# Performance work log

Hardware: AMD Instinct MI355X
Metric: run time of the kernel (lower is better)

Reference implementation:

```python
import jax, jax.numpy as jnp
import numpy as np

N_ATOMS = 50000
N_EDGES = 600000
N_FEAT = 128      # n_atom_basis
N_FILT = 128      # n_filters
N_GAUSS = 32
N_CONV = 3
CUTOFF = 5.0
ATOMS_PER_MOL = 50
N_MOL = N_ATOMS // ATOMS_PER_MOL
N_KEYS = 2        # energy_0, energy_1
HIDDEN_RO = 64
LOG2 = float(np.log(2.0))


def ssp(x):
    # shifted softplus: softplus(x) - log(2)
    return jax.nn.softplus(x) - LOG2


def setup_inputs() -> dict:
    key = jax.random.key(0)
    ks = jax.random.split(key, 16)
    def w(k, shape, fan_in):
        return jax.random.normal(k, shape, dtype=jnp.float32) / np.sqrt(fan_in)
    return {
        "z": jax.random.randint(ks[0], (N_ATOMS,), 1, 100),
        "xyz": jax.random.normal(ks[1], (N_ATOMS, 3), dtype=jnp.float32) * 4.0,
        "nbr_list": jax.random.randint(ks[2], (N_EDGES, 2), 0, N_ATOMS),
        "mol_idx": jnp.arange(N_ATOMS, dtype=jnp.int32) // ATOMS_PER_MOL,
        "embed": jax.random.normal(ks[3], (100, N_FEAT), dtype=jnp.float32) * 0.1,
        "We1": w(ks[4], (N_CONV, N_GAUSS, N_FILT), N_GAUSS),
        "be1": jnp.zeros((N_CONV, N_FILT), jnp.float32),
        "We2": w(ks[5], (N_CONV, N_FILT, N_FILT), N_FILT),
        "be2": jnp.zeros((N_CONV, N_FILT), jnp.float32),
        "Wn": w(ks[6], (N_CONV, N_FEAT, N_FILT), N_FEAT),
        "bn": jnp.zeros((N_CONV, N_FILT), jnp.float32),
        "Wu1": w(ks[7], (N_CONV, N_FILT, N_FEAT), N_FILT),
        "bu1": jnp.zeros((N_CONV, N_FEAT), jnp.float32),
        "Wu2": w(ks[8], (N_CONV, N_FEAT, N_FEAT), N_FEAT),
        "bu2": jnp.zeros((N_CONV, N_FEAT), jnp.float32),
        "Wr1": w(ks[9], (N_KEYS, N_FEAT, HIDDEN_RO), N_FEAT),
        "br1": jnp.zeros((N_KEYS, HIDDEN_RO), jnp.float32),
        "Wr2": w(ks[10], (N_KEYS, HIDDEN_RO, 1), HIDDEN_RO),
        "br2": jnp.zeros((N_KEYS, 1), jnp.float32),
    }


def _forward(xyz, embed, We1, be1, We2, be2, Wn, bn, Wu1, bu1, Wu2, bu2,
             Wr1, br1, Wr2, br2, z, nbr_list, mol_idx):
    a0, a1 = nbr_list[:, 0], nbr_list[:, 1]
    # pairwise distances e = ||xyz_i - xyz_j||  -> [E,1]
    diff = xyz[a0] - xyz[a1]
    d = jnp.sqrt(jnp.sum(diff * diff, axis=1, keepdims=True))
    # Gaussian smearing on [0, cutoff]
    offs = jnp.linspace(0.0, CUTOFF, N_GAUSS).astype(xyz.dtype)
    width = offs[1] - offs[0]
    gauss = jnp.exp((-0.5 / (width * width)) * (d - offs[None, :]) ** 2)  # [E,G]
    r = embed[z]  # [N,F] atom embedding lookup
    for l in range(N_CONV):
        # edge filter MLP: G -> Filt -> Filt
        ef = ssp(gauss @ We1[l] + be1[l]) @ We2[l] + be2[l]       # [E,Filt]
        rf = r @ Wn[l] + bn[l]                                    # [N,Filt]
        m_ij = rf[a0] * ef                                        # gather * filter
        m_ji = rf[a1] * ef
        agg = (jax.ops.segment_sum(m_ij, a1, num_segments=N_ATOMS)
               + jax.ops.segment_sum(m_ji, a0, num_segments=N_ATOMS))
        # update MLP, residual add
        r = r + (ssp(agg @ Wu1[l] + bu1[l]) @ Wu2[l] + bu2[l])
    # per-key atomwise readout: F -> H -> 1
    h = ssp(jnp.einsum('nf,kfh->knh', r, Wr1) + br1[:, None, :])          # [K,N,H]
    e_atom = (jnp.einsum('knh,kho->kno', h, Wr2) + br2[:, None, :])[..., 0]  # [K,N]
    # sum atom energies per molecule (batch_and_sum)
    e_mol = jax.ops.segment_sum(e_atom.T, mol_idx, num_segments=N_MOL)    # [M,K]
    return e_mol


def reference(z, xyz, nbr_list, mol_idx, embed, We1, be1, We2, be2, Wn, bn,
              Wu1, bu1, Wu2, bu2, Wr1, br1, Wr2, br2):
    return _forward(xyz, embed, We1, be1, We2, be2, Wn, bn, Wu1, bu1,
                    Wu2, bu2, Wr1, br1, Wr2, br2, z, nbr_list, mol_idx)
```

## Files before the change

kernel.cpp:

```cpp
#include <hip/hip_runtime.h>
#include <math.h>

#define N_ATOMS   50000
#define N_PAD     50048
#define N_EDGES   600000
#define N_FEAT    128
#define N_GAUSS   32
#define N_CONV    3
#define N_MOLS    1000
#define HIDDEN_RO 64
#define CAP       64

#define TBL_N     7681
#define TBL_BPL   121
#define TBL_SCALE 1024.0f
#define TBL_TMAX  7679.0f
#define NB_EDGE   2344
#define NB_BUILD  (N_CONV * TBL_BPL)
#define NB_EMBG   7
#define NB_WPREP  40

typedef unsigned int   uint32;
typedef unsigned short u16;
typedef __attribute__((ext_vector_type(8))) short bf16x8;
typedef __attribute__((ext_vector_type(4))) float f32x4;

__device__ __forceinline__ float ssp_f(float x) {
    float e = __expf(-fabsf(x));
    return fmaxf(x, 0.0f) + __logf(1.0f + e) - 0.6931471805599453f;
}
__device__ __forceinline__ uint32 f2bf_u(float x) {
    uint32 u = __float_as_uint(x);
    return (u + 0x7fffu + ((u >> 16) & 1u)) >> 16;
}
__device__ __forceinline__ uint32 pack2f(float a, float b) {
    return f2bf_u(a) | (f2bf_u(b) << 16);
}
__device__ __forceinline__ float bf_lo(uint32 u) { return __uint_as_float(u << 16); }
__device__ __forceinline__ float bf_hi(uint32 u) { return __uint_as_float(u & 0xffff0000u); }

__global__ __launch_bounds__(256)
void k_uberA(const int* __restrict__ nbr, const float* __restrict__ xyz,
             int* __restrict__ cnt, uint32* __restrict__ inc32,
             const float* __restrict__ We1_all, const float* __restrict__ be1_all,
             const float* __restrict__ We2_all, const float* __restrict__ be2_all,
             uint32* __restrict__ tblI,
             const float* __restrict__ Wn, const float* __restrict__ bn,
             const float* __restrict__ Wu1,
             const float* __restrict__ Wu2, const float* __restrict__ Wr1,
             u16* __restrict__ Wt, const float* __restrict__ embed,
             float* __restrict__ Gp) {
    __shared__ float smemA[26112 / 4];
    int b = blockIdx.x;
    int t = threadIdx.x;

    if (b < NB_BUILD) {
        int l    = b / TBL_BPL;
        int row0 = (b % TBL_BPL) * 64;
        const float* We1 = We1_all + (size_t)l * N_GAUSS * N_FEAT;
        const float* be1 = be1_all + (size_t)l * N_FEAT;
        const float* We2 = We2_all + (size_t)l * N_FEAT * N_FEAT;
        const float* be2 = be2_all + (size_t)l * N_FEAT;
        uint32* tl = tblI + (size_t)l * TBL_N * 128;
        float (*gT)[68] = (float(*)[68])smemA;
        u16* h1T = (u16*)(smemA + 32 * 68);

        const float width = 5.0f / 31.0f;
        const float coef = -0.5f / (width * width);
        #pragma unroll
        for (int i = 0; i < 8; ++i) {
            int idx = t + 256 * i;
            int g = idx >> 6, e = idx & 63;
            float d = (float)(row0 + e) * (1.0f / TBL_SCALE);
            float diff = d - (float)g * width;
            gT[g][e] = __expf(coef * diff * diff);
        }
        __syncthreads();

        int tf = t & 15, te = t >> 4;
        int f0 = tf * 8, eb = te * 4;
        float acc[4][8];
        #pragma unroll
        for (int i = 0; i < 4; ++i)
            #pragma unroll
            for (int j = 0; j < 8; ++j) acc[i][j] = 0.0f;

        #pragma unroll 4
        for (int g = 0; g < N_GAUSS; ++g) {
            float4 a  = *(const float4*)&gT[g][eb];
            float4 w0 = *(const float4*)(We1 + g * N_FEAT + f0);
            float4 w1 = *(const float4*)(We1 + g * N_FEAT + f0 + 4);
            float av[4] = {a.x, a.y, a.z, a.w};
            float wv[8] = {w0.x, w0.y, w0.z, w0.w, w1.x, w1.y, w1.z, w1.w};
            #pragma unroll
            for (int i = 0; i < 4; ++i)
                #pragma unroll
                for (int j = 0; j < 8; ++j) acc[i][j] += av[i] * wv[j];
        }
        #pragma unroll
        for (int j = 0; j < 8; ++j) {
            float bb2 = be1[f0 + j];
            uint2 hv;
            hv.x = pack2f(ssp_f(acc[0][j] + bb2), ssp_f(acc[1][j] + bb2));
            hv.y = pack2f(ssp_f(acc[2][j] + bb2), ssp_f(acc[3][j] + bb2));
            *(uint2*)&h1T[(f0 + j) * 68 + eb] = hv;
        }
        __syncthreads();

        #pragma unroll
        for (int i = 0; i < 4; ++i)
            #pragma unroll
            for (int j = 0; j < 8; ++j) acc[i][j] = 0.0f;
        #pragma unroll 2
        for (int c = 0; c < N_FEAT; ++c) {
            uint2 hv = *(const uint2*)&h1T[c * 68 + eb];
            float av[4] = {bf_lo(hv.x), bf_hi(hv.x), bf_lo(hv.y), bf_hi(hv.y)};
            float4 w0 = *(const float4*)(We2 + c * N_FEAT + f0);
            float4 w1 = *(const float4*)(We2 + c * N_FEAT + f0 + 4);
            float wv[8] = {w0.x, w0.y, w0.z, w0.w, w1.x, w1.y, w1.z, w1.w};
            #pragma unroll
            for (int i = 0; i < 4; ++i)
                #pragma unroll
                for (int j = 0; j < 8; ++j) acc[i][j] += av[i] * wv[j];
        }
        __syncthreads();

        uint32* pvS = (uint32*)smemA;
        #pragma unroll
        for (int i = 0; i < 4; ++i)
            #pragma unroll
            for (int p = 0; p < 4; ++p)
                pvS[(eb + i) * 65 + tf * 4 + p] =
                    pack2f(acc[i][2 * p]     + be2[f0 + 2 * p],
                           acc[i][2 * p + 1] + be2[f0 + 2 * p + 1]);
        __syncthreads();

        #pragma unroll
        for (int i = 0; i < 16; ++i) {
            int idx = t + 256 * i;
            int e = idx >> 6, fp = idx & 63;
            int ent = row0 + e;
            if (ent < TBL_N - 1) {
                if (e < 63) {
                    uint2 v2;
                    v2.x = pvS[e * 65 + fp];
                    v2.y = pvS[(e + 1) * 65 + fp];
                    *(uint2*)(tl + ((size_t)ent * 64 + fp) * 2) = v2;
                } else {
                    tl[((size_t)ent * 64 + fp) * 2] = pvS[63 * 65 + fp];
                }
            }
        }
        if (row0 > 0 && t < 64)
            tl[((size_t)(row0 - 1) * 64 + t) * 2 + 1] = pvS[t];
        return;
    }
    if (b < NB_BUILD + NB_EMBG) {
        int bb = b - NB_BUILD;
        int row = bb * 16 + (t >> 4);
        int tf = t & 15;
        if (row < 100) {
            float acc[8];
            #pragma unroll
            for (int j = 0; j < 8; ++j) acc[j] = 0.0f;
            for (int k = 0; k < N_FEAT; ++k) {
                float a = embed[row * N_FEAT + k];
                float4 w0 = *(const float4*)(Wn + k * N_FEAT + tf * 8);
                float4 w1 = *(const float4*)(Wn + k * N_FEAT + tf * 8 + 4);
                acc[0] += a * w0.x; acc[1] += a * w0.y;
                acc[2] += a * w0.z; acc[3] += a * w0.w;
                acc[4] += a * w1.x; acc[5] += a * w1.y;
                acc[6] += a * w1.z; acc[7] += a * w1.w;
            }
            #pragma unroll
            for (int j = 0; j < 8; ++j)
                Gp[row * N_FEAT + tf * 8 + j] = acc[j] + bn[tf * 8 + j];
        }
        return;
    }
    if (b < NB_BUILD + NB_EMBG + NB_WPREP) {
        int wb = b - NB_BUILD - NB_EMBG;
        int gid = wb * 256 + t;
        #pragma unroll
        for (int i = 0; i < 16; ++i) {
            int idx = gid + i * (NB_WPREP * 256);
            int mat = idx >> 14;
            int e = idx & 16383;
            int n = e >> 7, k = e & 127;
            float v;
            if (mat < 3)      v = Wn [(size_t)mat * 16384 + k * 128 + n];
            else if (mat < 6) v = Wu1[(size_t)(mat - 3) * 16384 + k * 128 + n];
            else if (mat < 9) v = Wu2[(size_t)(mat - 6) * 16384 + k * 128 + n];
            else { int key = n >> 6, h = n & 63; v = Wr1[(size_t)key * 128 * 64 + k * 64 + h]; }
            Wt[(size_t)mat * 16384 + n * 128 + k] = (u16)f2bf_u(v);
        }
        return;
    }
    {
        int e = (b - NB_BUILD - NB_EMBG - NB_WPREP) * 256 + t;
        if (e < N_EDGES) {
            int a0 = nbr[2 * e], a1 = nbr[2 * e + 1];
            float dx = xyz[3 * a0]     - xyz[3 * a1];
            float dy = xyz[3 * a0 + 1] - xyz[3 * a1 + 1];
            float dz = xyz[3 * a0 + 2] - xyz[3 * a1 + 2];
            float d = sqrtf(dx * dx + dy * dy + dz * dz);
            float tv = fminf(d * TBL_SCALE, TBL_TMAX);
            uint32 tq = (uint32)(tv * 8.0f + 0.5f);
            int p1 = atomicAdd(&cnt[a1], 1);
            if (p1 < CAP) inc32[((size_t)a1 << 6) | p1] = ((uint32)a0 << 16) | tq;
            int p0 = atomicAdd(&cnt[a0], 1);
            if (p0 < CAP) inc32[((size_t)a0 << 6) | p0] = ((uint32)a1 << 16) | tq;
        }
    }
}

__global__ __launch_bounds__(256)
void k_gather(const int* __restrict__ z, const float* __restrict__ embed,
              const float* __restrict__ Gp, float* __restrict__ r,
              uint32* __restrict__ rf16) {
    int idx = blockIdx.x * 256 + threadIdx.x;
    if (idx >= N_PAD * 32) return;
    int n = idx >> 5, c4 = idx & 31;
    int zz = z[n < N_ATOMS ? n : 0];
    float4 v = *(const float4*)(embed + (size_t)zz * N_FEAT + c4 * 4);
    *(float4*)(r + (size_t)n * N_FEAT + c4 * 4) = v;
    float4 g = *(const float4*)(Gp + (size_t)zz * N_FEAT + c4 * 4);
    uint2 o;
    o.x = pack2f(g.x, g.y);
    o.y = pack2f(g.z, g.w);
    *(uint2*)(rf16 + (size_t)n * 64 + c4 * 2) = o;
}

__global__ __launch_bounds__(256)
void k_agg(const int* __restrict__ cnt, const uint32* __restrict__ inc32,
           const uint32* __restrict__ tblI, const uint32* __restrict__ rf,
           uint32* __restrict__ agg16) {
    int wv = threadIdx.x >> 6, lane = threadIdx.x & 63;
    int h = lane >> 5, lh = lane & 31;
    int n = blockIdx.x * 4 + wv;
    if (n >= N_ATOMS) return;
    int s = n << 6;
    int e = s + min(cnt[n], CAP);
    float a0 = 0.f, a1 = 0.f, a2 = 0.f, a3 = 0.f;
    int i = s;
    for (; i + 8 <= e; i += 8) {
        uint32 v[4];
        #pragma unroll
        for (int u = 0; u < 4; ++u) v[u] = inc32[i + 2 * u + h];
        int i0[4], oa[4];
        float fr[4];
        #pragma unroll
        for (int u = 0; u < 4; ++u) {
            oa[u] = v[u] >> 16;
            uint32 tq = v[u] & 0xffffu;
            i0[u] = tq >> 3;
            fr[u] = (float)(tq & 7u) * 0.125f;
        }
        uint4 T[4];
        #pragma unroll
        for (int u = 0; u < 4; ++u) T[u] = *(const uint4*)(tblI + ((size_t)i0[u] * 64 + lh * 2) * 2);
        uint2 R[4];
        #pragma unroll
        for (int u = 0; u < 4; ++u) R[u] = *(const uint2*)(rf + (size_t)oa[u] * 64 + lh * 2);
        #pragma unroll
        for (int u = 0; u < 4; ++u) {
            float e0 = fmaf(fr[u], bf_lo(T[u].y) - bf_lo(T[u].x), bf_lo(T[u].x));
            float e1 = fmaf(fr[u], bf_hi(T[u].y) - bf_hi(T[u].x), bf_hi(T[u].x));
            float e2 = fmaf(fr[u], bf_lo(T[u].w) - bf_lo(T[u].z), bf_lo(T[u].z));
            float e3 = fmaf(fr[u], bf_hi(T[u].w) - bf_hi(T[u].z), bf_hi(T[u].z));
            a0 = fmaf(e0, bf_lo(R[u].x), a0);
            a1 = fmaf(e1, bf_hi(R[u].x), a1);
            a2 = fmaf(e2, bf_lo(R[u].y), a2);
            a3 = fmaf(e3, bf_hi(R[u].y), a3);
        }
    }
    for (; i < e; i += 2) {
        int idx = i + h;
        bool ok = idx < e;
        uint32 v = inc32[ok ? idx : s];
        int oa = v >> 16;
        uint32 tq = v & 0xffffu;
        int i0 = tq >> 3;
        float fr = (float)(tq & 7u) * 0.125f;
        uint4 T = *(const uint4*)(tblI + ((size_t)i0 * 64 + lh * 2) * 2);
        uint2 R = *(const uint2*)(rf + (size_t)oa * 64 + lh * 2);
        float m = ok ? 1.0f : 0.0f;
        float e0 = fmaf(fr, bf_lo(T.y) - bf_lo(T.x), bf_lo(T.x));
        float e1 = fmaf(fr, bf_hi(T.y) - bf_hi(T.x), bf_hi(T.x));
        float e2 = fmaf(fr, bf_lo(T.w) - bf_lo(T.z), bf_lo(T.z));
        float e3 = fmaf(fr, bf_hi(T.w) - bf_hi(T.z), bf_hi(T.z));
        a0 = fmaf(e0, m * bf_lo(R.x), a0);
        a1 = fmaf(e1, m * bf_hi(R.x), a1);
        a2 = fmaf(e2, m * bf_lo(R.y), a2);
        a3 = fmaf(e3, m * bf_hi(R.y), a3);
    }
    a0 += __shfl_xor(a0, 32);
    a1 += __shfl_xor(a1, 32);
    a2 += __shfl_xor(a2, 32);
    a3 += __shfl_xor(a3, 32);
    if (h == 0) {
        uint2 o;
        o.x = pack2f(a0, a1);
        o.y = pack2f(a2, a3);
        *(uint2*)(agg16 + (size_t)n * 64 + lh * 2) = o;
    }
}

template <bool RO>
__global__ __launch_bounds__(256)
void k_update(const u16* __restrict__ agg16u,
              const float* __restrict__ bu1, const float* __restrict__ bu2,
              const u16* __restrict__ Wu1t, const u16* __restrict__ Wu2t,
              const u16* __restrict__ W3t, const float* __restrict__ b3,
              float* __restrict__ r, u16* __restrict__ rf16,
              const float* __restrict__ Wr2, const float* __restrict__ br2,
              const int* __restrict__ mol, float* __restrict__ out) {
    __shared__ u16 aT[32 * 136];
    __shared__ u16 hT[32 * 136];

    int tid = threadIdx.x;
    int w = tid >> 6, lane = tid & 63;
    int l15 = lane & 15, q = lane >> 4;
    int colbase = w * 32;
    size_t n0 = (size_t)blockIdx.x * 32;

    bf16x8 bfr[4][2];
    #pragma unroll
    for (int kc = 0; kc < 4; ++kc)
        #pragma unroll
        for (int ntl = 0; ntl < 2; ++ntl)
            bfr[kc][ntl] = *(const bf16x8*)(Wu1t + (size_t)(colbase + ntl * 16 + l15) * 128 + kc * 32 + q * 8);
    float rpre[2][2][4];
    #pragma unroll
    for (int ntl = 0; ntl < 2; ++ntl) {
        int col = colbase + ntl * 16 + l15;
        #pragma unroll
        for (int m = 0; m < 2; ++m)
            #pragma unroll
            for (int reg = 0; reg < 4; ++reg)
                rpre[ntl][m][reg] = r[(n0 + m * 16 + q * 4 + reg) * N_FEAT + col];
    }

    #pragma unroll
    for (int i = 0; i < 2; ++i) {
        int idx = tid + 256 * i;
        int row = idx >> 4, c = idx & 15;
        uint4 v = *(const uint4*)(agg16u + (n0 + row) * 128 + c * 8);
        *(uint4*)&aT[row * 136 + c * 8] = v;
    }
    __syncthreads();

    f32x4 acc[2][2];

    #pragma unroll
    for (int m = 0; m < 2; ++m)
        #pragma unroll
        for (int ntl = 0; ntl < 2; ++ntl) acc[m][ntl] = (f32x4){0.f, 0.f, 0.f, 0.f};
    #pragma unroll
    for (int kc = 0; kc < 4; ++kc)
        #pragma unroll
        for (int m = 0; m < 2; ++m) {
            bf16x8 a = *(const bf16x8*)(aT + (m * 16 + l15) * 136 + kc * 32 + q * 8);
            acc[m][0] = __builtin_amdgcn_mfma_f32_16x16x32_bf16(a, bfr[kc][0], acc[m][0], 0, 0, 0);
            acc[m][1] = __builtin_amdgcn_mfma_f32_16x16x32_bf16(a, bfr[kc][1], acc[m][1], 0, 0, 0);
        }
    #pragma unroll
    for (int ntl = 0; ntl < 2; ++ntl) {
        int col = colbase + ntl * 16 + l15;
        float bv = bu1[col];
        #pragma unroll
        for (int m = 0; m < 2; ++m)
            #pragma unroll
            for (int reg = 0; reg < 4; ++reg)
                hT[(m * 16 + q * 4 + reg) * 136 + col] = (u16)f2bf_u(ssp_f(acc[m][ntl][reg] + bv));
    }
    __syncthreads();

    #pragma unroll
    for (int kc = 0; kc < 4; ++kc)
        #pragma unroll
        for (int ntl = 0; ntl < 2; ++ntl)
            bfr[kc][ntl] = *(const bf16x8*)(Wu2t + (size_t)(colbase + ntl * 16 + l15) * 128 + kc * 32 + q * 8);
    #pragma unroll
    for (int m = 0; m < 2; ++m)
        #pragma unroll
        for (int ntl = 0; ntl < 2; ++ntl) acc[m][ntl] = (f32x4){0.f, 0.f, 0.f, 0.f};
    #pragma unroll
    for (int kc = 0; kc < 4; ++kc)
        #pragma unroll
        for (int m = 0; m < 2; ++m) {
            bf16x8 a = *(const bf16x8*)(hT + (m * 16 + l15) * 136 + kc * 32 + q * 8);
            acc[m][0] = __builtin_amdgcn_mfma_f32_16x16x32_bf16(a, bfr[kc][0], acc[m][0], 0, 0, 0);
            acc[m][1] = __builtin_amdgcn_mfma_f32_16x16x32_bf16(a, bfr[kc][1], acc[m][1], 0, 0, 0);
        }
    __syncthreads();
    #pragma unroll
    for (int ntl = 0; ntl < 2; ++ntl) {
        int col = colbase + ntl * 16 + l15;
        float bv = bu2[col];
        #pragma unroll
        for (int m = 0; m < 2; ++m)
            #pragma unroll
            for (int reg = 0; reg < 4; ++reg) {
                int row = m * 16 + q * 4 + reg;
                float v = acc[m][ntl][reg] + bv + rpre[ntl][m][reg];
                if (!RO) r[(n0 + row) * N_FEAT + col] = v;
                aT[row * 136 + col] = (u16)f2bf_u(v);
            }
    }
    __syncthreads();

    #pragma unroll
    for (int kc = 0; kc < 4; ++kc)
        #pragma unroll
        for (int ntl = 0; ntl < 2; ++ntl)
            bfr[kc][ntl] = *(const bf16x8*)(W3t + (size_t)(colbase + ntl * 16 + l15) * 128 + kc * 32 + q * 8);
    #pragma unroll
    for (int m = 0; m < 2; ++m)
        #pragma unroll
        for (int ntl = 0; ntl < 2; ++ntl) acc[m][ntl] = (f32x4){0.f, 0.f, 0.f, 0.f};
    #pragma unroll
    for (int kc = 0; kc < 4; ++kc)
        #pragma unroll
        for (int m = 0; m < 2; ++m) {
            bf16x8 a = *(const bf16x8*)(aT + (m * 16 + l15) * 136 + kc * 32 + q * 8);
            acc[m][0] = __builtin_amdgcn_mfma_f32_16x16x32_bf16(a, bfr[kc][0], acc[m][0], 0, 0, 0);
            acc[m][1] = __builtin_amdgcn_mfma_f32_16x16x32_bf16(a, bfr[kc][1], acc[m][1], 0, 0, 0);
        }

    if (!RO) {
        #pragma unroll
        for (int ntl = 0; ntl < 2; ++ntl) {
            int col = colbase + ntl * 16 + l15;
            float bv = b3[col];
            #pragma unroll
            for (int m = 0; m < 2; ++m)
                #pragma unroll
                for (int reg = 0; reg < 4; ++reg) {
                    int row = m * 16 + q * 4 + reg;
                    rf16[(n0 + row) * N_FEAT + col] = (u16)f2bf_u(acc[m][ntl][reg] + bv);
                }
        }
    } else {
        float (*red)[4][17] = (float(*)[4][17])aT;
        __syncthreads();
        float b1v[2], w2v[2];
        #pragma unroll
        for (int ntl = 0; ntl < 2; ++ntl) {
            int col = colbase + ntl * 16 + l15;
            b1v[ntl] = b3[col];
            w2v[ntl] = Wr2[col];
        }
        #pragma unroll
        for (int m = 0; m < 2; ++m)
            #pragma unroll
            for (int reg = 0; reg < 4; ++reg) {
                float pk = ssp_f(acc[m][0][reg] + b1v[0]) * w2v[0]
                         + ssp_f(acc[m][1][reg] + b1v[1]) * w2v[1];
                red[m * 16 + q * 4 + reg][w][l15] = pk;
            }
        __syncthreads();
        if (tid < 64) {
            int row = tid & 31, key = tid >> 5;
            int atom = (int)n0 + row;
            if (atom < N_ATOMS) {
                float s = br2[key];
                #pragma unroll
                for (int j = 0; j < 16; ++j)
                    s += red[row][2 * key][j] + red[row][2 * key + 1][j];
                atomicAdd(&out[mol[atom] * 2 + key], s);
            }
        }
    }
}

extern "C" void kernel_launch(void* const* d_in, const int* in_sizes, int n_in,
                              void* d_out, int out_size, void* d_ws, size_t ws_size,
                              hipStream_t stream) {
    const int*   z     = (const int*)d_in[0];
    const float* xyz   = (const float*)d_in[1];
    const int*   nbr   = (const int*)d_in[2];
    const int*   mol   = (const int*)d_in[3];
    const float* embed = (const float*)d_in[4];
    const float* We1   = (const float*)d_in[5];
    const float* be1   = (const float*)d_in[6];
    const float* We2   = (const float*)d_in[7];
    const float* be2   = (const float*)d_in[8];
    const float* Wn    = (const float*)d_in[9];
    const float* bn    = (const float*)d_in[10];
    const float* Wu1   = (const float*)d_in[11];
    const float* bu1   = (const float*)d_in[12];
    const float* Wu2   = (const float*)d_in[13];
    const float* bu2   = (const float*)d_in[14];
    const float* Wr1   = (const float*)d_in[15];
    const float* br1   = (const float*)d_in[16];
    const float* Wr2   = (const float*)d_in[17];
    const float* br2   = (const float*)d_in[18];
    float* out = (float*)d_out;

    float* ws = (float*)d_ws;
    const size_t NRP = (size_t)N_PAD * N_FEAT;
    const size_t NHP = (size_t)N_PAD * 64;
    float*  r_buf  = ws;
    uint32* agg16  = (uint32*)(ws + NRP);
    uint32* rf16   = agg16 + NHP;
    int*    cnt    = (int*)(rf16 + NHP);
    uint32* inc32  = (uint32*)(cnt + 50048);
    uint32* tblI   = inc32 + (size_t)N_ATOMS * CAP;
    u16*    Wt     = (u16*)(tblI + (size_t)3 * TBL_N * 128);
    float*  Gp     = (float*)(Wt + 10 * 16384);

    hipMemsetAsync(d_out, 0, (size_t)out_size * sizeof(float), stream);
    hipMemsetAsync(cnt, 0, 50000 * sizeof(int), stream);

    k_uberA<<<NB_BUILD + NB_EMBG + NB_WPREP + NB_EDGE, 256, 0, stream>>>(
        nbr, xyz, cnt, inc32, We1, be1, We2, be2, tblI,
        Wn, bn, Wu1, Wu2, Wr1, Wt, embed, Gp);

    k_gather<<<(N_PAD * 32) / 256, 256, 0, stream>>>(z, embed, Gp, r_buf, rf16);

    const int GA2 = N_PAD / 32;
    for (int l = 0; l < N_CONV; ++l) {
        k_agg<<<(N_ATOMS + 3) / 4, 256, 0, stream>>>(cnt, inc32,
                                                     tblI + (size_t)l * TBL_N * 128,
                                                     rf16, agg16);
        const u16* Wu1t = Wt + (size_t)(3 + l) * 16384;
        const u16* Wu2t = Wt + (size_t)(6 + l) * 16384;
        if (l < N_CONV - 1) {
            k_update<false><<<GA2, 256, 0, stream>>>((const u16*)agg16, bu1 + l * 128,
                                                     bu2 + l * 128, Wu1t, Wu2t,
                                                     Wt + (size_t)(l + 1) * 16384,
                                                     bn + (l + 1) * 128,
                                                     r_buf, (u16*)rf16, Wr2, br2, mol, out);
        } else {
            k_update<true><<<GA2, 256, 0, stream>>>((const u16*)agg16, bu1 + l * 128,
                                                    bu2 + l * 128, Wu1t, Wu2t,
                                                    Wt + (size_t)9 * 16384, br1,
                                                    r_buf, (u16*)rf16, Wr2, br2, mol, out);
        }
    }
}
```

Baseline: 468.7 us.

## Partition edge fill by atom class and shrink update tile to 16 rows

The edge-fill stage now has each block scan 2048 edges and handle only the endpoints whose atom index falls in one of eight residue classes (b & 7). Atomics and incidence writes to a given atom therefore come from a subset of blocks, which is meant to reduce atomic contention and scattered writes, at the cost of reading every edge eight times and recomputing distances. Separately, the update kernel processes 16 atoms per block instead of 32, doubling the grid and halving per-block register and LDS use to raise occupancy. In exchange, each block loads the weight fragments for only half as many rows.

New measurement: 489.4 us. +4.4%, slower.

```diff
diff --git a/kernel.cpp b/kernel.cpp
--- a/kernel.cpp
+++ b/kernel.cpp
@@ -39,6 +39,7 @@
 __device__ __forceinline__ float bf_lo(uint32 u) { return __uint_as_float(u << 16); }
 __device__ __forceinline__ float bf_hi(uint32 u) { return __uint_as_float(u & 0xffff0000u); }
 
+#define FILL_START (NB_BUILD + NB_EMBG + NB_WPREP)
 __global__ __launch_bounds__(256)
 void k_uberA(const int* __restrict__ nbr, const float* __restrict__ xyz,
              int* __restrict__ cnt, uint32* __restrict__ inc32,
@@ -178,7 +179,7 @@
         }
         return;
     }
-    if (b < NB_BUILD + NB_EMBG + NB_WPREP) {
+    if (b < FILL_START) {
         int wb = b - NB_BUILD - NB_EMBG;
         int gid = wb * 256 + t;
         #pragma unroll
@@ -197,19 +198,31 @@
         return;
     }
     {
-        int e = (b - NB_BUILD - NB_EMBG - NB_WPREP) * 256 + t;
-        if (e < N_EDGES) {
-            int a0 = nbr[2 * e], a1 = nbr[2 * e + 1];
-            float dx = xyz[3 * a0]     - xyz[3 * a1];
-            float dy = xyz[3 * a0 + 1] - xyz[3 * a1 + 1];
-            float dz = xyz[3 * a0 + 2] - xyz[3 * a1 + 2];
-            float d = sqrtf(dx * dx + dy * dy + dz * dz);
-            float tv = fminf(d * TBL_SCALE, TBL_TMAX);
-            uint32 tq = (uint32)(tv * 8.0f + 0.5f);
-            int p1 = atomicAdd(&cnt[a1], 1);
-            if (p1 < CAP) inc32[((size_t)a1 << 6) | p1] = ((uint32)a0 << 16) | tq;
-            int p0 = atomicAdd(&cnt[a0], 1);
-            if (p0 < CAP) inc32[((size_t)a0 << 6) | p0] = ((uint32)a1 << 16) | tq;
+        int cls = b & 7;
+        int base = ((b - FILL_START) >> 3) * 2048;
+        #pragma unroll
+        for (int i = 0; i < 8; ++i) {
+            int e = base + t + 256 * i;
+            if (e < N_EDGES) {
+                int a0 = nbr[2 * e], a1 = nbr[2 * e + 1];
+                bool m0 = (a0 & 7) == cls, m1 = (a1 & 7) == cls;
+                if (m0 | m1) {
+                    float dx = xyz[3 * a0]     - xyz[3 * a1];
+                    float dy = xyz[3 * a0 + 1] - xyz[3 * a1 + 1];
+                    float dz = xyz[3 * a0 + 2] - xyz[3 * a1 + 2];
+                    float d = sqrtf(dx * dx + dy * dy + dz * dz);
+                    float tv = fminf(d * TBL_SCALE, TBL_TMAX);
+                    uint32 tq = (uint32)(tv * 8.0f + 0.5f);
+                    if (m1) {
+                        int p1 = atomicAdd(&cnt[a1], 1);
+                        if (p1 < CAP) inc32[((size_t)a1 << 6) | p1] = ((uint32)a0 << 16) | tq;
+                    }
+                    if (m0) {
+                        int p0 = atomicAdd(&cnt[a0], 1);
+                        if (p0 < CAP) inc32[((size_t)a0 << 6) | p0] = ((uint32)a1 << 16) | tq;
+                    }
+                }
+            }
         }
     }
 }
@@ -315,14 +328,14 @@
               float* __restrict__ r, u16* __restrict__ rf16,
               const float* __restrict__ Wr2, const float* __restrict__ br2,
               const int* __restrict__ mol, float* __restrict__ out) {
-    __shared__ u16 aT[32 * 136];
-    __shared__ u16 hT[32 * 136];
+    __shared__ u16 aT[16 * 136];
+    __shared__ u16 hT[16 * 136];
 
     int tid = threadIdx.x;
     int w = tid >> 6, lane = tid & 63;
     int l15 = lane & 15, q = lane >> 4;
     int colbase = w * 32;
-    size_t n0 = (size_t)blockIdx.x * 32;
+    size_t n0 = (size_t)blockIdx.x * 16;
 
     bf16x8 bfr[4][2];
     #pragma unroll
@@ -330,49 +343,39 @@
         #pragma unroll
         for (int ntl = 0; ntl < 2; ++ntl)
             bfr[kc][ntl] = *(const bf16x8*)(Wu1t + (size_t)(colbase + ntl * 16 + l15) * 128 + kc * 32 + q * 8);
-    float rpre[2][2][4];
+    float rpre[2][4];
     #pragma unroll
     for (int ntl = 0; ntl < 2; ++ntl) {
         int col = colbase + ntl * 16 + l15;
         #pragma unroll
-        for (int m = 0; m < 2; ++m)
-            #pragma unroll
-            for (int reg = 0; reg < 4; ++reg)
-                rpre[ntl][m][reg] = r[(n0 + m * 16 + q * 4 + reg) * N_FEAT + col];
-    }
-
-    #pragma unroll
-    for (int i = 0; i < 2; ++i) {
-        int idx = tid + 256 * i;
-        int row = idx >> 4, c = idx & 15;
+        for (int reg = 0; reg < 4; ++reg)
+            rpre[ntl][reg] = r[(n0 + q * 4 + reg) * N_FEAT + col];
+    }
+
+    {
+        int row = tid >> 4, c = tid & 15;
         uint4 v = *(const uint4*)(agg16u + (n0 + row) * 128 + c * 8);
         *(uint4*)&aT[row * 136 + c * 8] = v;
     }
     __syncthreads();
 
-    f32x4 acc[2][2];
-
-    #pragma unroll
-    for (int m = 0; m < 2; ++m)
-        #pragma unroll
-        for (int ntl = 0; ntl < 2; ++ntl) acc[m][ntl] = (f32x4){0.f, 0.f, 0.f, 0.f};
-    #pragma unroll
-    for (int kc = 0; kc < 4; ++kc)
-        #pragma unroll
-        for (int m = 0; m < 2; ++m) {
-            bf16x8 a = *(const bf16x8*)(aT + (m * 16 + l15) * 136 + kc * 32 + q * 8);
-            acc[m][0] = __builtin_amdgcn_mfma_f32_16x16x32_bf16(a, bfr[kc][0], acc[m][0], 0, 0, 0);
-            acc[m][1] = __builtin_amdgcn_mfma_f32_16x16x32_bf16(a, bfr[kc][1], acc[m][1], 0, 0, 0);
-        }
+    f32x4 acc[2];
+
+    acc[0] = (f32x4){0.f, 0.f, 0.f, 0.f};
+    acc[1] = (f32x4){0.f, 0.f, 0.f, 0.f};
+    #pragma unroll
+    for (int kc = 0; kc < 4; ++kc) {
+        bf16x8 a = *(const bf16x8*)(aT + l15 * 136 + kc * 32 + q * 8);
+        acc[0] = __builtin_amdgcn_mfma_f32_16x16x32_bf16(a, bfr[kc][0], acc[0], 0, 0, 0);
+        acc[1] = __builtin_amdgcn_mfma_f32_16x16x32_bf16(a, bfr[kc][1], acc[1], 0, 0, 0);
+    }
     #pragma unroll
     for (int ntl = 0; ntl < 2; ++ntl) {
         int col = colbase + ntl * 16 + l15;
         float bv = bu1[col];
         #pragma unroll
-        for (int m = 0; m < 2; ++m)
-            #pragma unroll
-            for (int reg = 0; reg < 4; ++reg)
-                hT[(m * 16 + q * 4 + reg) * 136 + col] = (u16)f2bf_u(ssp_f(acc[m][ntl][reg] + bv));
+        for (int reg = 0; reg < 4; ++reg)
+            hT[(q * 4 + reg) * 136 + col] = (u16)f2bf_u(ssp_f(acc[ntl][reg] + bv));
     }
     __syncthreads();
 
@@ -381,32 +384,26 @@
         #pragma unroll
         for (int ntl = 0; ntl < 2; ++ntl)
             bfr[kc][ntl] = *(const bf16x8*)(Wu2t + (size_t)(colbase + ntl * 16 + l15) * 128 + kc * 32 + q * 8);
-    #pragma unroll
-    for (int m = 0; m < 2; ++m)
-        #pragma unroll
-        for (int ntl = 0; ntl < 2; ++ntl) acc[m][ntl] = (f32x4){0.f, 0.f, 0.f, 0.f};
-    #pragma unroll
-    for (int kc = 0; kc < 4; ++kc)
-        #pragma unroll
-        for (int m = 0; m < 2; ++m) {
-            bf16x8 a = *(const bf16x8*)(hT + (m * 16 + l15) * 136 + kc * 32 + q * 8);
-            acc[m][0] = __builtin_amdgcn_mfma_f32_16x16x32_bf16(a, bfr[kc][0], acc[m][0], 0, 0, 0);
-            acc[m][1] = __builtin_amdgcn_mfma_f32_16x16x32_bf16(a, bfr[kc][1], acc[m][1], 0, 0, 0);
-        }
+    acc[0] = (f32x4){0.f, 0.f, 0.f, 0.f};
+    acc[1] = (f32x4){0.f, 0.f, 0.f, 0.f};
+    #pragma unroll
+    for (int kc = 0; kc < 4; ++kc) {
+        bf16x8 a = *(const bf16x8*)(hT + l15 * 136 + kc * 32 + q * 8);
+        acc[0] = __builtin_amdgcn_mfma_f32_16x16x32_bf16(a, bfr[kc][0], acc[0], 0, 0, 0);
+        acc[1] = __builtin_amdgcn_mfma_f32_16x16x32_bf16(a, bfr[kc][1], acc[1], 0, 0, 0);
+    }
     __syncthreads();
     #pragma unroll
     for (int ntl = 0; ntl < 2; ++ntl) {
         int col = colbase + ntl * 16 + l15;
         float bv = bu2[col];
         #pragma unroll
-        for (int m = 0; m < 2; ++m)
-            #pragma unroll
-            for (int reg = 0; reg < 4; ++reg) {
-                int row = m * 16 + q * 4 + reg;
-                float v = acc[m][ntl][reg] + bv + rpre[ntl][m][reg];
-                if (!RO) r[(n0 + row) * N_FEAT + col] = v;
-                aT[row * 136 + col] = (u16)f2bf_u(v);
-            }
+        for (int reg = 0; reg < 4; ++reg) {
+            int row = q * 4 + reg;
+            float v = acc[ntl][reg] + bv + rpre[ntl][reg];
+            if (!RO) r[(n0 + row) * N_FEAT + col] = v;
+            aT[row * 136 + col] = (u16)f2bf_u(v);
+        }
     }
     __syncthreads();
 
@@ -415,18 +412,14 @@
         #pragma unroll
         for (int ntl = 0; ntl < 2; ++ntl)
             bfr[kc][ntl] = *(const bf16x8*)(W3t + (size_t)(colbase + ntl * 16 + l15) * 128 + kc * 32 + q * 8);
-    #pragma unroll
-    for (int m = 0; m < 2; ++m)
-        #pragma unroll
-        for (int ntl = 0; ntl < 2; ++ntl) acc[m][ntl] = (f32x4){0.f, 0.f, 0.f, 0.f};
-    #pragma unroll
-    for (int kc = 0; kc < 4; ++kc)
-        #pragma unroll
-        for (int m = 0; m < 2; ++m) {
-            bf16x8 a = *(const bf16x8*)(aT + (m * 16 + l15) * 136 + kc * 32 + q * 8);
-            acc[m][0] = __builtin_amdgcn_mfma_f32_16x16x32_bf16(a, bfr[kc][0], acc[m][0], 0, 0, 0);
-            acc[m][1] = __builtin_amdgcn_mfma_f32_16x16x32_bf16(a, bfr[kc][1], acc[m][1], 0, 0, 0);
-        }
+    acc[0] = (f32x4){0.f, 0.f, 0.f, 0.f};
+    acc[1] = (f32x4){0.f, 0.f, 0.f, 0.f};
+    #pragma unroll
+    for (int kc = 0; kc < 4; ++kc) {
+        bf16x8 a = *(const bf16x8*)(aT + l15 * 136 + kc * 32 + q * 8);
+        acc[0] = __builtin_amdgcn_mfma_f32_16x16x32_bf16(a, bfr[kc][0], acc[0], 0, 0, 0);
+        acc[1] = __builtin_amdgcn_mfma_f32_16x16x32_bf16(a, bfr[kc][1], acc[1], 0, 0, 0);
+    }
 
     if (!RO) {
         #pragma unroll
@@ -434,12 +427,10 @@
             int col = colbase + ntl * 16 + l15;
             float bv = b3[col];
             #pragma unroll
-            for (int m = 0; m < 2; ++m)
-                #pragma unroll
-                for (int reg = 0; reg < 4; ++reg) {
-                    int row = m * 16 + q * 4 + reg;
-                    rf16[(n0 + row) * N_FEAT + col] = (u16)f2bf_u(acc[m][ntl][reg] + bv);
-                }
+            for (int reg = 0; reg < 4; ++reg) {
+                int row = q * 4 + reg;
+                rf16[(n0 + row) * N_FEAT + col] = (u16)f2bf_u(acc[ntl][reg] + bv);
+            }
         }
     } else {
         float (*red)[4][17] = (float(*)[4][17])aT;
@@ -452,16 +443,14 @@
             w2v[ntl] = Wr2[col];
         }
         #pragma unroll
-        for (int m = 0; m < 2; ++m)
-            #pragma unroll
-            for (int reg = 0; reg < 4; ++reg) {
-                float pk = ssp_f(acc[m][0][reg] + b1v[0]) * w2v[0]
-                         + ssp_f(acc[m][1][reg] + b1v[1]) * w2v[1];
-                red[m * 16 + q * 4 + reg][w][l15] = pk;
-            }
+        for (int reg = 0; reg < 4; ++reg) {
+            float pk = ssp_f(acc[0][reg] + b1v[0]) * w2v[0]
+                     + ssp_f(acc[1][reg] + b1v[1]) * w2v[1];
+            red[q * 4 + reg][w][l15] = pk;
+        }
         __syncthreads();
-        if (tid < 64) {
-            int row = tid & 31, key = tid >> 5;
+        if (tid < 32) {
+            int row = tid & 15, key = tid >> 4;
             int atom = (int)n0 + row;
             if (atom < N_ATOMS) {
                 float s = br2[key];
@@ -513,13 +502,13 @@
     hipMemsetAsync(d_out, 0, (size_t)out_size * sizeof(float), stream);
     hipMemsetAsync(cnt, 0, 50000 * sizeof(int), stream);
 
-    k_uberA<<<NB_BUILD + NB_EMBG + NB_WPREP + NB_EDGE, 256, 0, stream>>>(
+    k_uberA<<<FILL_START + NB_EDGE, 256, 0, stream>>>(
         nbr, xyz, cnt, inc32, We1, be1, We2, be2, tblI,
         Wn, bn, Wu1, Wu2, Wr1, Wt, embed, Gp);
 
     k_gather<<<(N_PAD * 32) / 256, 256, 0, stream>>>(z, embed, Gp, r_buf, rf16);
 
-    const int GA2 = N_PAD / 32;
+    const int GA3 = N_PAD / 16;
     for (int l = 0; l < N_CONV; ++l) {
         k_agg<<<(N_ATOMS + 3) / 4, 256, 0, stream>>>(cnt, inc32,
                                                      tblI + (size_t)l * TBL_N * 128,
@@ -527,13 +516,13 @@
         const u16* Wu1t = Wt + (size_t)(3 + l) * 16384;
         const u16* Wu2t = Wt + (size_t)(6 + l) * 16384;
         if (l < N_CONV - 1) {
-            k_update<false><<<GA2, 256, 0, stream>>>((const u16*)agg16, bu1 + l * 128,
+            k_update<false><<<GA3, 256, 0, stream>>>((const u16*)agg16, bu1 + l * 128,
                                                      bu2 + l * 128, Wu1t, Wu2t,
                                                      Wt + (size_t)(l + 1) * 16384,
                                                      bn + (l + 1) * 128,
                                                      r_buf, (u16*)rf16, Wr2, br2, mol, out);
         } else {
-            k_update<true><<<GA2, 256, 0, stream>>>((const u16*)agg16, bu1 + l * 128,
+            k_update<true><<<GA3, 256, 0, stream>>>((const u16*)agg16, bu1 + l * 128,
                                                     bu2 + l * 128, Wu1t, Wu2t,
                                                     Wt + (size_t)9 * 16384, br1,
                                                     r_buf, (u16*)rf16, Wr2, br2, mol, out);
```

## Fuse edge aggregation into layer update kernel and partition edge fill by atom class

Applied to the files above, without the earlier changes.

The per-layer aggregation kernel is merged into the update kernel. Each block now aggregates its 32 atoms directly into shared memory, which removes the global agg16 round trip and one launch per layer. Because other blocks read rf while this one writes it, rf is double-buffered (ping-pong) to avoid read/write races. The edge-fill section now has each block scan 2048 edges and handle only the atoms whose index mod 8 matches the block's class. This spreads atomics across blocks so each class's atomics localize, but every edge is read 8 times and the fused kernel launches only about 1564 blocks, which lowers gather parallelism.

After: 503.6 us. +7.4%, slower.

```diff
diff --git a/kernel.cpp b/kernel.cpp
--- a/kernel.cpp
+++ b/kernel.cpp
@@ -39,6 +39,7 @@
 __device__ __forceinline__ float bf_lo(uint32 u) { return __uint_as_float(u << 16); }
 __device__ __forceinline__ float bf_hi(uint32 u) { return __uint_as_float(u & 0xffff0000u); }
 
+#define FILL_START (NB_BUILD + NB_EMBG + NB_WPREP)
 __global__ __launch_bounds__(256)
 void k_uberA(const int* __restrict__ nbr, const float* __restrict__ xyz,
              int* __restrict__ cnt, uint32* __restrict__ inc32,
@@ -178,7 +179,7 @@
         }
         return;
     }
-    if (b < NB_BUILD + NB_EMBG + NB_WPREP) {
+    if (b < FILL_START) {
         int wb = b - NB_BUILD - NB_EMBG;
         int gid = wb * 256 + t;
         #pragma unroll
@@ -197,19 +198,31 @@
         return;
     }
     {
-        int e = (b - NB_BUILD - NB_EMBG - NB_WPREP) * 256 + t;
-        if (e < N_EDGES) {
-            int a0 = nbr[2 * e], a1 = nbr[2 * e + 1];
-            float dx = xyz[3 * a0]     - xyz[3 * a1];
-            float dy = xyz[3 * a0 + 1] - xyz[3 * a1 + 1];
-            float dz = xyz[3 * a0 + 2] - xyz[3 * a1 + 2];
-            float d = sqrtf(dx * dx + dy * dy + dz * dz);
-            float tv = fminf(d * TBL_SCALE, TBL_TMAX);
-            uint32 tq = (uint32)(tv * 8.0f + 0.5f);
-            int p1 = atomicAdd(&cnt[a1], 1);
-            if (p1 < CAP) inc32[((size_t)a1 << 6) | p1] = ((uint32)a0 << 16) | tq;
-            int p0 = atomicAdd(&cnt[a0], 1);
-            if (p0 < CAP) inc32[((size_t)a0 << 6) | p0] = ((uint32)a1 << 16) | tq;
+        int cls = b & 7;
+        int base = ((b - FILL_START) >> 3) * 2048;
+        #pragma unroll
+        for (int i = 0; i < 8; ++i) {
+            int e = base + t + 256 * i;
+            if (e < N_EDGES) {
+                int a0 = nbr[2 * e], a1 = nbr[2 * e + 1];
+                bool m0 = (a0 & 7) == cls, m1 = (a1 & 7) == cls;
+                if (m0 | m1) {
+                    float dx = xyz[3 * a0]     - xyz[3 * a1];
+                    float dy = xyz[3 * a0 + 1] - xyz[3 * a1 + 1];
+                    float dz = xyz[3 * a0 + 2] - xyz[3 * a1 + 2];
+                    float d = sqrtf(dx * dx + dy * dy + dz * dz);
+                    float tv = fminf(d * TBL_SCALE, TBL_TMAX);
+                    uint32 tq = (uint32)(tv * 8.0f + 0.5f);
+                    if (m1) {
+                        int p1 = atomicAdd(&cnt[a1], 1);
+                        if (p1 < CAP) inc32[((size_t)a1 << 6) | p1] = ((uint32)a0 << 16) | tq;
+                    }
+                    if (m0) {
+                        int p0 = atomicAdd(&cnt[a0], 1);
+                        if (p0 < CAP) inc32[((size_t)a0 << 6) | p0] = ((uint32)a1 << 16) | tq;
+                    }
+                }
+            }
         }
     }
 }
@@ -231,90 +244,16 @@
     *(uint2*)(rf16 + (size_t)n * 64 + c4 * 2) = o;
 }
 
-__global__ __launch_bounds__(256)
-void k_agg(const int* __restrict__ cnt, const uint32* __restrict__ inc32,
-           const uint32* __restrict__ tblI, const uint32* __restrict__ rf,
-           uint32* __restrict__ agg16) {
-    int wv = threadIdx.x >> 6, lane = threadIdx.x & 63;
-    int h = lane >> 5, lh = lane & 31;
-    int n = blockIdx.x * 4 + wv;
-    if (n >= N_ATOMS) return;
-    int s = n << 6;
-    int e = s + min(cnt[n], CAP);
-    float a0 = 0.f, a1 = 0.f, a2 = 0.f, a3 = 0.f;
-    int i = s;
-    for (; i + 8 <= e; i += 8) {
-        uint32 v[4];
-        #pragma unroll
-        for (int u = 0; u < 4; ++u) v[u] = inc32[i + 2 * u + h];
-        int i0[4], oa[4];
-        float fr[4];
-        #pragma unroll
-        for (int u = 0; u < 4; ++u) {
-            oa[u] = v[u] >> 16;
-            uint32 tq = v[u] & 0xffffu;
-            i0[u] = tq >> 3;
-            fr[u] = (float)(tq & 7u) * 0.125f;
-        }
-        uint4 T[4];
-        #pragma unroll
-        for (int u = 0; u < 4; ++u) T[u] = *(const uint4*)(tblI + ((size_t)i0[u] * 64 + lh * 2) * 2);
-        uint2 R[4];
-        #pragma unroll
-        for (int u = 0; u < 4; ++u) R[u] = *(const uint2*)(rf + (size_t)oa[u] * 64 + lh * 2);
-        #pragma unroll
-        for (int u = 0; u < 4; ++u) {
-            float e0 = fmaf(fr[u], bf_lo(T[u].y) - bf_lo(T[u].x), bf_lo(T[u].x));
-            float e1 = fmaf(fr[u], bf_hi(T[u].y) - bf_hi(T[u].x), bf_hi(T[u].x));
-            float e2 = fmaf(fr[u], bf_lo(T[u].w) - bf_lo(T[u].z), bf_lo(T[u].z));
-            float e3 = fmaf(fr[u], bf_hi(T[u].w) - bf_hi(T[u].z), bf_hi(T[u].z));
-            a0 = fmaf(e0, bf_lo(R[u].x), a0);
-            a1 = fmaf(e1, bf_hi(R[u].x), a1);
-            a2 = fmaf(e2, bf_lo(R[u].y), a2);
-            a3 = fmaf(e3, bf_hi(R[u].y), a3);
-        }
-    }
-    for (; i < e; i += 2) {
-        int idx = i + h;
-        bool ok = idx < e;
-        uint32 v = inc32[ok ? idx : s];
-        int oa = v >> 16;
-        uint32 tq = v & 0xffffu;
-        int i0 = tq >> 3;
-        float fr = (float)(tq & 7u) * 0.125f;
-        uint4 T = *(const uint4*)(tblI + ((size_t)i0 * 64 + lh * 2) * 2);
-        uint2 R = *(const uint2*)(rf + (size_t)oa * 64 + lh * 2);
-        float m = ok ? 1.0f : 0.0f;
-        float e0 = fmaf(fr, bf_lo(T.y) - bf_lo(T.x), bf_lo(T.x));
-        float e1 = fmaf(fr, bf_hi(T.y) - bf_hi(T.x), bf_hi(T.x));
-        float e2 = fmaf(fr, bf_lo(T.w) - bf_lo(T.z), bf_lo(T.z));
-        float e3 = fmaf(fr, bf_hi(T.w) - bf_hi(T.z), bf_hi(T.z));
-        a0 = fmaf(e0, m * bf_lo(R.x), a0);
-        a1 = fmaf(e1, m * bf_hi(R.x), a1);
-        a2 = fmaf(e2, m * bf_lo(R.y), a2);
-        a3 = fmaf(e3, m * bf_hi(R.y), a3);
-    }
-    a0 += __shfl_xor(a0, 32);
-    a1 += __shfl_xor(a1, 32);
-    a2 += __shfl_xor(a2, 32);
-    a3 += __shfl_xor(a3, 32);
-    if (h == 0) {
-        uint2 o;
-        o.x = pack2f(a0, a1);
-        o.y = pack2f(a2, a3);
-        *(uint2*)(agg16 + (size_t)n * 64 + lh * 2) = o;
-    }
-}
-
 template <bool RO>
 __global__ __launch_bounds__(256)
-void k_update(const u16* __restrict__ agg16u,
-              const float* __restrict__ bu1, const float* __restrict__ bu2,
-              const u16* __restrict__ Wu1t, const u16* __restrict__ Wu2t,
-              const u16* __restrict__ W3t, const float* __restrict__ b3,
-              float* __restrict__ r, u16* __restrict__ rf16,
-              const float* __restrict__ Wr2, const float* __restrict__ br2,
-              const int* __restrict__ mol, float* __restrict__ out) {
+void k_layer(const int* __restrict__ cnt, const uint32* __restrict__ inc32,
+             const uint32* __restrict__ tblI, const uint32* __restrict__ rf_in,
+             const float* __restrict__ bu1, const float* __restrict__ bu2,
+             const u16* __restrict__ Wu1t, const u16* __restrict__ Wu2t,
+             const u16* __restrict__ W3t, const float* __restrict__ b3,
+             float* __restrict__ r, u16* __restrict__ rf_out,
+             const float* __restrict__ Wr2, const float* __restrict__ br2,
+             const int* __restrict__ mol, float* __restrict__ out) {
     __shared__ u16 aT[32 * 136];
     __shared__ u16 hT[32 * 136];
 
@@ -324,6 +263,82 @@
     int colbase = w * 32;
     size_t n0 = (size_t)blockIdx.x * 32;
 
+    {
+        int h = lane >> 5, lh = lane & 31;
+        for (int ai = 0; ai < 8; ++ai) {
+            int row = w * 8 + ai;
+            int n = (int)n0 + row;
+            float a0 = 0.f, a1 = 0.f, a2 = 0.f, a3 = 0.f;
+            if (n < N_ATOMS) {
+                int s = n << 6;
+                int e = s + min(cnt[n], CAP);
+                int i = s;
+                for (; i + 8 <= e; i += 8) {
+                    uint32 v[4];
+                    #pragma unroll
+                    for (int u = 0; u < 4; ++u) v[u] = inc32[i + 2 * u + h];
+                    int i0[4], oa[4];
+                    float fr[4];
+                    #pragma unroll
+                    for (int u = 0; u < 4; ++u) {
+                        oa[u] = v[u] >> 16;
+                        uint32 tq = v[u] & 0xffffu;
+                        i0[u] = tq >> 3;
+                        fr[u] = (float)(tq & 7u) * 0.125f;
+                    }
+                    uint4 T[4];
+                    #pragma unroll
+                    for (int u = 0; u < 4; ++u) T[u] = *(const uint4*)(tblI + ((size_t)i0[u] * 64 + lh * 2) * 2);
+                    uint2 R[4];
+                    #pragma unroll
+                    for (int u = 0; u < 4; ++u) R[u] = *(const uint2*)(rf_in + (size_t)oa[u] * 64 + lh * 2);
+                    #pragma unroll
+                    for (int u = 0; u < 4; ++u) {
+                        float e0 = fmaf(fr[u], bf_lo(T[u].y) - bf_lo(T[u].x), bf_lo(T[u].x));
+                        float e1 = fmaf(fr[u], bf_hi(T[u].y) - bf_hi(T[u].x), bf_hi(T[u].x));
+                        float e2 = fmaf(fr[u], bf_lo(T[u].w) - bf_lo(T[u].z), bf_lo(T[u].z));
+                        float e3 = fmaf(fr[u], bf_hi(T[u].w) - bf_hi(T[u].z), bf_hi(T[u].z));
+                        a0 = fmaf(e0, bf_lo(R[u].x), a0);
+                        a1 = fmaf(e1, bf_hi(R[u].x), a1);
+                        a2 = fmaf(e2, bf_lo(R[u].y), a2);
+                        a3 = fmaf(e3, bf_hi(R[u].y), a3);
+                    }
+                }
+                for (; i < e; i += 2) {
+                    int idx = i + h;
+                    bool ok = idx < e;
+                    uint32 v = inc32[ok ? idx : s];
+                    int oa = v >> 16;
+                    uint32 tq = v & 0xffffu;
+                    int i0 = tq >> 3;
+                    float fr = (float)(tq & 7u) * 0.125f;
+                    uint4 T = *(const uint4*)(tblI + ((size_t)i0 * 64 + lh * 2) * 2);
+                    uint2 R = *(const uint2*)(rf_in + (size_t)oa * 64 + lh * 2);
+                    float m = ok ? 1.0f : 0.0f;
+                    float e0 = fmaf(fr, bf_lo(T.y) - bf_lo(T.x), bf_lo(T.x));
+                    float e1 = fmaf(fr, bf_hi(T.y) - bf_hi(T.x), bf_hi(T.x));
+                    float e2 = fmaf(fr, bf_lo(T.w) - bf_lo(T.z), bf_lo(T.z));
+                    float e3 = fmaf(fr, bf_hi(T.w) - bf_hi(T.z), bf_hi(T.z));
+                    a0 = fmaf(e0, m * bf_lo(R.x), a0);
+                    a1 = fmaf(e1, m * bf_hi(R.x), a1);
+                    a2 = fmaf(e2, m * bf_lo(R.y), a2);
+                    a3 = fmaf(e3, m * bf_hi(R.y), a3);
+                }
+                a0 += __shfl_xor(a0, 32);
+                a1 += __shfl_xor(a1, 32);
+                a2 += __shfl_xor(a2, 32);
+                a3 += __shfl_xor(a3, 32);
+            }
+            if (h == 0) {
+                uint2 o;
+                o.x = pack2f(a0, a1);
+                o.y = pack2f(a2, a3);
+                *(uint2*)&aT[row * 136 + lh * 4] = o;
+            }
+        }
+    }
+    __syncthreads();
+
     bf16x8 bfr[4][2];
     #pragma unroll
     for (int kc = 0; kc < 4; ++kc)
@@ -340,15 +355,6 @@
             for (int reg = 0; reg < 4; ++reg)
                 rpre[ntl][m][reg] = r[(n0 + m * 16 + q * 4 + reg) * N_FEAT + col];
     }
-
-    #pragma unroll
-    for (int i = 0; i < 2; ++i) {
-        int idx = tid + 256 * i;
-        int row = idx >> 4, c = idx & 15;
-        uint4 v = *(const uint4*)(agg16u + (n0 + row) * 128 + c * 8);
-        *(uint4*)&aT[row * 136 + c * 8] = v;
-    }
-    __syncthreads();
 
     f32x4 acc[2][2];
 
@@ -438,7 +444,7 @@
                 #pragma unroll
                 for (int reg = 0; reg < 4; ++reg) {
                     int row = m * 16 + q * 4 + reg;
-                    rf16[(n0 + row) * N_FEAT + col] = (u16)f2bf_u(acc[m][ntl][reg] + bv);
+                    rf_out[(n0 + row) * N_FEAT + col] = (u16)f2bf_u(acc[m][ntl][reg] + bv);
                 }
         }
     } else {
@@ -502,9 +508,9 @@
     const size_t NRP = (size_t)N_PAD * N_FEAT;
     const size_t NHP = (size_t)N_PAD * 64;
     float*  r_buf  = ws;
-    uint32* agg16  = (uint32*)(ws + NRP);
-    uint32* rf16   = agg16 + NHP;
-    int*    cnt    = (int*)(rf16 + NHP);
+    uint32* rfA    = (uint32*)(ws + NRP);
+    uint32* rfB    = rfA + NHP;
+    int*    cnt    = (int*)(rfB + NHP);
     uint32* inc32  = (uint32*)(cnt + 50048);
     uint32* tblI   = inc32 + (size_t)N_ATOMS * CAP;
     u16*    Wt     = (u16*)(tblI + (size_t)3 * TBL_N * 128);
@@ -513,30 +519,32 @@
     hipMemsetAsync(d_out, 0, (size_t)out_size * sizeof(float), stream);
     hipMemsetAsync(cnt, 0, 50000 * sizeof(int), stream);
 
-    k_uberA<<<NB_BUILD + NB_EMBG + NB_WPREP + NB_EDGE, 256, 0, stream>>>(
+    k_uberA<<<FILL_START + NB_EDGE, 256, 0, stream>>>(
         nbr, xyz, cnt, inc32, We1, be1, We2, be2, tblI,
         Wn, bn, Wu1, Wu2, Wr1, Wt, embed, Gp);
 
-    k_gather<<<(N_PAD * 32) / 256, 256, 0, stream>>>(z, embed, Gp, r_buf, rf16);
-
-    const int GA2 = N_PAD / 32;
+    k_gather<<<(N_PAD * 32) / 256, 256, 0, stream>>>(z, embed, Gp, r_buf, rfA);
+
+    const int GL = N_PAD / 32;
+    uint32* rin = rfA;
+    uint32* rout = rfB;
     for (int l = 0; l < N_CONV; ++l) {
-        k_agg<<<(N_ATOMS + 3) / 4, 256, 0, stream>>>(cnt, inc32,
-                                                     tblI + (size_t)l * TBL_N * 128,
-                                                     rf16, agg16);
         const u16* Wu1t = Wt + (size_t)(3 + l) * 16384;
         const u16* Wu2t = Wt + (size_t)(6 + l) * 16384;
         if (l < N_CONV - 1) {
-            k_update<false><<<GA2, 256, 0, stream>>>((const u16*)agg16, bu1 + l * 128,
-                                                     bu2 + l * 128, Wu1t, Wu2t,
-                                                     Wt + (size_t)(l + 1) * 16384,
-                                                     bn + (l + 1) * 128,
-                                                     r_buf, (u16*)rf16, Wr2, br2, mol, out);
+            k_layer<false><<<GL, 256, 0, stream>>>(cnt, inc32,
+                                                   tblI + (size_t)l * TBL_N * 128, rin,
+                                                   bu1 + l * 128, bu2 + l * 128, Wu1t, Wu2t,
+                                                   Wt + (size_t)(l + 1) * 16384,
+                                                   bn + (l + 1) * 128,
+                                                   r_buf, (u16*)rout, Wr2, br2, mol, out);
         } else {
-            k_update<true><<<GA2, 256, 0, stream>>>((const u16*)agg16, bu1 + l * 128,
-                                                    bu2 + l * 128, Wu1t, Wu2t,
-                                                    Wt + (size_t)9 * 16384, br1,
-                                                    r_buf, (u16*)rf16, Wr2, br2, mol, out);
-        }
-    }
-}
+            k_layer<true><<<GL, 256, 0, stream>>>(cnt, inc32,
+                                                  tblI + (size_t)l * TBL_N * 128, rin,
+                                                  bu1 + l * 128, bu2 + l * 128, Wu1t, Wu2t,
+                                                  Wt + (size_t)9 * 16384, br1,
+                                                  r_buf, (u16*)rout, Wr2, br2, mol, out);
+        }
+        uint32* tmp = rin; rin = rout; rout = tmp;
+    }
+}
```

## Prepack weights in MFMA fragment order and partition edge fill by atom class

Applied to the files above, without the earlier changes.

The weight-prep stage now writes the bf16 transposed weights directly in the per-lane MFMA B-fragment order. k_update can then load each weight fragment as one contiguous 16-byte chunk per lane, instead of strided row reads. The edge-fill stage now has each group of 8 consecutive blocks scan the same 2048 edges. Each block handles only edges whose endpoint satisfies atom & 7 == block & 7, which keeps the atomic counters and incidence writes for a given atom class within blocks likely scheduled on the same XCD. The cost is that neighbor indices and coordinates are re-read up to 8 times, and per-block work is less balanced.

Result: faster. 429.5 us (-8.4%).

```diff
diff --git a/kernel.cpp b/kernel.cpp
--- a/kernel.cpp
+++ b/kernel.cpp
@@ -39,6 +39,8 @@
 __device__ __forceinline__ float bf_lo(uint32 u) { return __uint_as_float(u << 16); }
 __device__ __forceinline__ float bf_hi(uint32 u) { return __uint_as_float(u & 0xffff0000u); }
 
+
+#define FILL_START (NB_BUILD + NB_EMBG + NB_WPREP)
 __global__ __launch_bounds__(256)
 void k_uberA(const int* __restrict__ nbr, const float* __restrict__ xyz,
              int* __restrict__ cnt, uint32* __restrict__ inc32,
@@ -178,38 +180,54 @@
         }
         return;
     }
-    if (b < NB_BUILD + NB_EMBG + NB_WPREP) {
+    if (b < FILL_START) {
         int wb = b - NB_BUILD - NB_EMBG;
         int gid = wb * 256 + t;
         #pragma unroll
         for (int i = 0; i < 16; ++i) {
             int idx = gid + i * (NB_WPREP * 256);
-            int mat = idx >> 14;
-            int e = idx & 16383;
-            int n = e >> 7, k = e & 127;
+            int j    = idx & 7;
+            int lane = (idx >> 3) & 63;
+            int cg   = (idx >> 9) & 7;
+            int kc   = (idx >> 12) & 3;
+            int mat  = idx >> 14;
+            int col  = cg * 16 + (lane & 15);
+            int k    = kc * 32 + (lane >> 4) * 8 + j;
             float v;
-            if (mat < 3)      v = Wn [(size_t)mat * 16384 + k * 128 + n];
-            else if (mat < 6) v = Wu1[(size_t)(mat - 3) * 16384 + k * 128 + n];
-            else if (mat < 9) v = Wu2[(size_t)(mat - 6) * 16384 + k * 128 + n];
-            else { int key = n >> 6, h = n & 63; v = Wr1[(size_t)key * 128 * 64 + k * 64 + h]; }
-            Wt[(size_t)mat * 16384 + n * 128 + k] = (u16)f2bf_u(v);
+            if (mat < 3)      v = Wn [(size_t)mat * 16384 + k * 128 + col];
+            else if (mat < 6) v = Wu1[(size_t)(mat - 3) * 16384 + k * 128 + col];
+            else if (mat < 9) v = Wu2[(size_t)(mat - 6) * 16384 + k * 128 + col];
+            else { int key = col >> 6, h = col & 63; v = Wr1[(size_t)key * 128 * 64 + k * 64 + h]; }
+            Wt[(size_t)idx] = (u16)f2bf_u(v);
         }
         return;
     }
     {
-        int e = (b - NB_BUILD - NB_EMBG - NB_WPREP) * 256 + t;
-        if (e < N_EDGES) {
-            int a0 = nbr[2 * e], a1 = nbr[2 * e + 1];
-            float dx = xyz[3 * a0]     - xyz[3 * a1];
-            float dy = xyz[3 * a0 + 1] - xyz[3 * a1 + 1];
-            float dz = xyz[3 * a0 + 2] - xyz[3 * a1 + 2];
-            float d = sqrtf(dx * dx + dy * dy + dz * dz);
-            float tv = fminf(d * TBL_SCALE, TBL_TMAX);
-            uint32 tq = (uint32)(tv * 8.0f + 0.5f);
-            int p1 = atomicAdd(&cnt[a1], 1);
-            if (p1 < CAP) inc32[((size_t)a1 << 6) | p1] = ((uint32)a0 << 16) | tq;
-            int p0 = atomicAdd(&cnt[a0], 1);
-            if (p0 < CAP) inc32[((size_t)a0 << 6) | p0] = ((uint32)a1 << 16) | tq;
+        int cls = b & 7;
+        int base = ((b - FILL_START) >> 3) * 2048;
+        #pragma unroll
+        for (int i = 0; i < 8; ++i) {
+            int e = base + t + 256 * i;
+            if (e < N_EDGES) {
+                int a0 = nbr[2 * e], a1 = nbr[2 * e + 1];
+                bool m0 = (a0 & 7) == cls, m1 = (a1 & 7) == cls;
+                if (m0 | m1) {
+                    float dx = xyz[3 * a0]     - xyz[3 * a1];
+                    float dy = xyz[3 * a0 + 1] - xyz[3 * a1 + 1];
+                    float dz = xyz[3 * a0 + 2] - xyz[3 * a1 + 2];
+                    float d = sqrtf(dx * dx + dy * dy + dz * dz);
+                    float tv = fminf(d * TBL_SCALE, TBL_TMAX);
+                    uint32 tq = (uint32)(tv * 8.0f + 0.5f);
+                    if (m1) {
+                        int p1 = atomicAdd(&cnt[a1], 1);
+                        if (p1 < CAP) inc32[((size_t)a1 << 6) | p1] = ((uint32)a0 << 16) | tq;
+                    }
+                    if (m0) {
+                        int p0 = atomicAdd(&cnt[a0], 1);
+                        if (p0 < CAP) inc32[((size_t)a0 << 6) | p0] = ((uint32)a1 << 16) | tq;
+                    }
+                }
+            }
         }
     }
 }
@@ -323,13 +341,14 @@
     int l15 = lane & 15, q = lane >> 4;
     int colbase = w * 32;
     size_t n0 = (size_t)blockIdx.x * 32;
+    size_t fragoff = (size_t)(w * 2) * 512 + (size_t)lane * 8;
 
     bf16x8 bfr[4][2];
     #pragma unroll
     for (int kc = 0; kc < 4; ++kc)
         #pragma unroll
         for (int ntl = 0; ntl < 2; ++ntl)
-            bfr[kc][ntl] = *(const bf16x8*)(Wu1t + (size_t)(colbase + ntl * 16 + l15) * 128 + kc * 32 + q * 8);
+            bfr[kc][ntl] = *(const bf16x8*)(Wu1t + kc * 4096 + ntl * 512 + fragoff);
     float rpre[2][2][4];
     #pragma unroll
     for (int ntl = 0; ntl < 2; ++ntl) {
@@ -380,7 +399,7 @@
     for (int kc = 0; kc < 4; ++kc)
         #pragma unroll
         for (int ntl = 0; ntl < 2; ++ntl)
-            bfr[kc][ntl] = *(const bf16x8*)(Wu2t + (size_t)(colbase + ntl * 16 + l15) * 128 + kc * 32 + q * 8);
+            bfr[kc][ntl] = *(const bf16x8*)(Wu2t + kc * 4096 + ntl * 512 + fragoff);
     #pragma unroll
     for (int m = 0; m < 2; ++m)
         #pragma unroll
@@ -414,7 +433,7 @@
     for (int kc = 0; kc < 4; ++kc)
         #pragma unroll
         for (int ntl = 0; ntl < 2; ++ntl)
-            bfr[kc][ntl] = *(const bf16x8*)(W3t + (size_t)(colbase + ntl * 16 + l15) * 128 + kc * 32 + q * 8);
+            bfr[kc][ntl] = *(const bf16x8*)(W3t + kc * 4096 + ntl * 512 + fragoff);
     #pragma unroll
     for (int m = 0; m < 2; ++m)
         #pragma unroll
@@ -513,7 +532,7 @@
     hipMemsetAsync(d_out, 0, (size_t)out_size * sizeof(float), stream);
     hipMemsetAsync(cnt, 0, 50000 * sizeof(int), stream);
 
-    k_uberA<<<NB_BUILD + NB_EMBG + NB_WPREP + NB_EDGE, 256, 0, stream>>>(
+    k_uberA<<<FILL_START + NB_EDGE, 256, 0, stream>>>(
         nbr, xyz, cnt, inc32, We1, be1, We2, be2, tblI,
         Wn, bn, Wu1, Wu2, Wr1, Wt, embed, Gp);
 
```
